# Performance work log

Hardware: AMD Instinct MI355X
Metric: run time of the kernel (lower is better)

The kernel has to match this reference:

```python
import jax, jax.numpy as jnp
import numpy as np

N = 100000
E = 400000
G = 2000  # number of graphs in batch
IN_DIM = 32
H = 192
L = 4
EPS = 1e-5


def setup_inputs() -> dict:
    key = jax.random.key(0)
    ks = jax.random.split(key, 20)
    x = jax.random.normal(ks[0], (N, IN_DIM), jnp.float32)
    edge_src = jax.random.randint(ks[1], (E,), 0, N, jnp.int32)
    edge_dst = jax.random.randint(ks[2], (E,), 0, N, jnp.int32)
    batch = jnp.sort(jax.random.randint(ks[3], (N,), 0, G, jnp.int32))
    s_in = 1.0 / np.sqrt(IN_DIM)
    s_h = 1.0 / np.sqrt(H)
    return {
        "x": x,
        "edge_src": edge_src,
        "edge_dst": edge_dst,
        "batch": batch,
        # layer 0 (in_dim -> H); weights stored [in, out]
        "Wrel0": jax.random.uniform(ks[4], (IN_DIM, H), jnp.float32, -s_in, s_in),
        "brel0": jax.random.uniform(ks[5], (H,), jnp.float32, -s_in, s_in),
        "Wroot0": jax.random.uniform(ks[6], (IN_DIM, H), jnp.float32, -s_in, s_in),
        # layers 1..3 stacked (H -> H)
        "Wrel": jax.random.uniform(ks[7], (L - 1, H, H), jnp.float32, -s_h, s_h),
        "brel": jax.random.uniform(ks[8], (L - 1, H), jnp.float32, -s_h, s_h),
        "Wroot": jax.random.uniform(ks[9], (L - 1, H, H), jnp.float32, -s_h, s_h),
        # batchnorm affine params for all 4 layers
        "gamma": jnp.ones((L, H), jnp.float32),
        "beta": jnp.zeros((L, H), jnp.float32),
        # head MLP and output
        "Wh1": jax.random.uniform(ks[10], (H, H), jnp.float32, -s_h, s_h),
        "bh1": jax.random.uniform(ks[11], (H,), jnp.float32, -s_h, s_h),
        "Wh2": jax.random.uniform(ks[12], (H, H), jnp.float32, -s_h, s_h),
        "bh2": jax.random.uniform(ks[13], (H,), jnp.float32, -s_h, s_h),
        "Wout": jax.random.uniform(ks[14], (H, 1), jnp.float32, -s_h, s_h),
        "bout": jax.random.uniform(ks[15], (1,), jnp.float32, -s_h, s_h),
    }


def _rel_conv(x, edge_src, edge_dst, Wrel, brel, Wroot):
    # message: lin_rel(x_j); applying the linear at node level first is the
    # same math as per-edge (linear commutes with gather) and cheaper.
    h = x @ Wrel + brel                      # [N, out]
    agg = jax.ops.segment_sum(h[edge_src], edge_dst, num_segments=N)
    return agg + x @ Wroot


def _bn_relu(h, g, b):
    # BatchNorm1d in training mode: batch stats over node dim, biased var
    mu = h.mean(axis=0)
    var = jnp.var(h, axis=0)
    h = (h - mu) * jax.lax.rsqrt(var + EPS) * g + b
    return jax.nn.relu(h)


def reference(x, edge_src, edge_dst, batch, Wrel0, brel0, Wroot0,
              Wrel, brel, Wroot, gamma, beta, Wh1, bh1, Wh2, bh2, Wout, bout):
    h = _bn_relu(_rel_conv(x, edge_src, edge_dst, Wrel0, brel0, Wroot0),
                 gamma[0], beta[0])
    for i in range(L - 1):
        h = _bn_relu(_rel_conv(h, edge_src, edge_dst, Wrel[i], brel[i], Wroot[i]),
                     gamma[i + 1], beta[i + 1])
    # global mean pool over graphs
    sums = jax.ops.segment_sum(h, batch, num_segments=G)          # [G, H]
    cnt = jax.ops.segment_sum(jnp.ones((N,), h.dtype), batch, num_segments=G)
    g = sums / jnp.maximum(cnt, 1.0)[:, None]
    # head MLP (dropout is identity at eval) + output linear
    g = jax.nn.relu(g @ Wh1 + bh1) @ Wh2 + bh2
    return g @ Wout + bout                                        # [G, 1]
```

## Files before the change

### kernel.cpp

```cpp
#include <hip/hip_runtime.h>

#define HDIM 192
#define EPS 1e-5f

typedef __attribute__((ext_vector_type(8))) _Float16 half8;
typedef __attribute__((ext_vector_type(4))) float floatx4;

__device__ __forceinline__ float h2f(ushort u) {
    union { ushort u; _Float16 h; } c; c.u = u; return (float)c.h;
}
__device__ __forceinline__ ushort f2h(float x) {
    _Float16 h = (_Float16)x;
    union { _Float16 h; ushort u; } c; c.h = h; return c.u;
}
__device__ __forceinline__ uint4 pack8(const ushort* h) {
    uint4 p;
    p.x = h[0] | ((uint)h[1] << 16); p.y = h[2] | ((uint)h[3] << 16);
    p.z = h[4] | ((uint)h[5] << 16); p.w = h[6] | ((uint)h[7] << 16);
    return p;
}

__device__ __forceinline__ void gload_lds16(const ushort* g, ushort* l) {
    __builtin_amdgcn_global_load_lds(
        (const __attribute__((address_space(1))) unsigned int*)g,
        (__attribute__((address_space(3))) unsigned int*)l, 16, 0, 0);
}

template<int M>
__device__ __forceinline__ void waitv() {
    if constexpr (M == 0)      asm volatile("s_waitcnt vmcnt(0)" ::: "memory");
    else if constexpr (M == 3) asm volatile("s_waitcnt vmcnt(3)" ::: "memory");
    else if constexpr (M == 7) asm volatile("s_waitcnt vmcnt(7)" ::: "memory");
    else                       asm volatile("s_waitcnt vmcnt(8)" ::: "memory");
}


struct PrepArgs {
    const float* src[6];
    ushort*      dst[6];
    int K[6];
    int off[7];
};

__global__ __launch_bounds__(256) void prep_all_k(PrepArgs a)
{
    int idx = blockIdx.x * 256 + threadIdx.x;
    if (idx >= a.off[6]) return;
    int i = 0;
    #pragma unroll
    for (int t = 1; t < 6; ++t) if (idx >= a.off[t]) i = t;
    int r = idx - a.off[i];
    int K = a.K[i];
    int perMat = (K >> 5) * 12 * 64;
    int mat = r / perMat;
    r -= mat * perMat;
    int lane = r & 63;
    int ct = (r >> 6) % 12;
    int kc = r / (12 * 64);
    int col = ct * 16 + (lane & 15);
    int kb  = kc * 32 + (lane >> 4) * 8;
    const float* Wm = a.src[i] + (size_t)mat * K * HDIM;
    ushort* base = a.dst[i] + (size_t)mat * K * HDIM;
    size_t o = (size_t)kc * 6144 + (size_t)(ct * 64 + lane) * 8;
    #pragma unroll
    for (int j = 0; j < 8; ++j)
        base[o + j] = f2h(Wm[(size_t)(kb + j) * HDIM + col]);
}

__global__ __launch_bounds__(256) void conv_half_k(
    const float* __restrict__ src, ushort* __restrict__ dst, int R, int C)
{
    int OC = C >> 3;
    int idx = blockIdx.x * 256 + threadIdx.x;
    if (idx >= R * OC) return;
    int r = idx / OC;
    int o = idx - r * OC;
    float4 v0 = ((const float4*)(src + (size_t)r * C + o * 8))[0];
    float4 v1 = ((const float4*)(src + (size_t)r * C + o * 8))[1];
    float v[8] = {v0.x, v0.y, v0.z, v0.w, v1.x, v1.y, v1.z, v1.w};
    ushort h[8];
    #pragma unroll
    for (int t = 0; t < 8; ++t) h[t] = f2h(v[t]);
    *(uint4*)(dst + (size_t)r * C + o * 8) = pack8(h);
}

template<bool DUAL, bool RELU, bool DEG, bool STATS, int NCH>
__global__ __launch_bounds__(256, 4) void gemm_mfma_k(
    const ushort* __restrict__ A1h, const ushort* __restrict__ W1f,
    const ushort* __restrict__ A2h, const ushort* __restrict__ W2f,
    const float* __restrict__ degf, const float* __restrict__ bias,
    ushort* __restrict__ C, float* __restrict__ stats, int N, int K)
{
    __shared__ float sstat[2][HDIM];
    __shared__ __align__(16) ushort smem[12800];
    const int tid  = threadIdx.x;
    const int wave = tid >> 6;
    const int lane = tid & 63;
    const int row0 = blockIdx.x * 64;
    const int m16 = lane & 15;
    const int g4  = lane >> 4;

    if (STATS && tid < HDIM) { sstat[0][tid] = 0.f; sstat[1][tid] = 0.f; }

    int srow = row0 + (tid >> 2); if (srow >= N) srow = N - 1;
    const size_t soff = (size_t)srow * K + (size_t)(tid & 3) * 8;

    const int nkc = K >> 5;

    auto stageA = [&](int c, int slot) {
        bool ph = DUAL && (c >= nkc);
        int kc = ph ? c - nkc : c;
        const ushort* g = (ph ? A2h : A1h) + soff + kc * 32;
        gload_lds16(g, smem + slot * 2048 + wave * 512);
    };
    auto loadB = [&](int c, half8* b) {
        bool ph = DUAL && (c >= nkc);
        int kc = ph ? c - nkc : c;
        const ushort* Bp = (ph ? W2f : W1f) + (size_t)kc * 6144
                         + (size_t)(wave * 192 + lane) * 8;
        #pragma unroll
        for (int ct = 0; ct < 3; ++ct)
            b[ct] = *(const half8*)(Bp + ct * 512);
    };

    floatx4 acc[4][3];
    #pragma unroll
    for (int s = 0; s < 4; ++s)
        #pragma unroll
        for (int ct = 0; ct < 3; ++ct) acc[s][ct] = (floatx4){0.f, 0.f, 0.f, 0.f};

    auto compute = [&](int slot, const half8* b) {
        const ushort* aB = smem + slot * 2048 + m16 * 32 + g4 * 8;
        half8 a[4];
        #pragma unroll
        for (int s = 0; s < 4; ++s)
            a[s] = *(const half8*)(aB + s * 512);
        #pragma unroll
        for (int ct = 0; ct < 3; ++ct)
            #pragma unroll
            for (int s = 0; s < 4; ++s)
                acc[s][ct] = __builtin_amdgcn_mfma_f32_16x16x32_f16(a[s], b[ct], acc[s][ct], 0, 0, 0);
    };

    half8 breg[3][3];
    stageA(0, 0); stageA(1, 1);
    if constexpr (NCH >= 3) stageA(2, 2);
    loadB(0, breg[0]); loadB(1, breg[1]);

    #pragma unroll
    for (int c = 0; c < NCH; ++c) {
        if (c + 3 < NCH) stageA(c + 3, (c + 3) % 5);
        if (c + 2 < NCH) loadB(c + 2, breg[(c + 2) % 3]);
        const int rem = NCH - 1 - c;
        if      (rem >= 3) waitv<8>();
        else if (rem == 2) waitv<7>();
        else if (rem == 1) waitv<3>();
        else               waitv<0>();
        __builtin_amdgcn_s_barrier();
        __builtin_amdgcn_sched_barrier(0);
        compute(c % 5, breg[c % 3]);
    }

    __syncthreads();
    #pragma unroll
    for (int ct = 0; ct < 3; ++ct) {
        int col = wave * 48 + ct * 16 + m16;
        float bv = bias ? bias[col] : 0.f;
        float lsum = 0.f, lsq = 0.f;
        #pragma unroll
        for (int s = 0; s < 4; ++s) {
            #pragma unroll
            for (int reg = 0; reg < 4; ++reg) {
                int rloc = s * 16 + g4 * 4 + reg;
                int rr = row0 + rloc;
                int rrc = rr < N ? rr : N - 1;
                float v = acc[s][ct][reg] + (DEG ? degf[rrc] * bv : bv);
                if (STATS && rr < N) { lsum += v; lsq += v * v; }
                if (RELU) v = fmaxf(v, 0.f);
                smem[rloc * 200 + col] = f2h(v);
            }
        }
        if (STATS) {
            lsum += __shfl_xor(lsum, 16); lsum += __shfl_xor(lsum, 32);
            lsq  += __shfl_xor(lsq, 16);  lsq  += __shfl_xor(lsq, 32);
            if (g4 == 0) {
                atomicAdd(&sstat[0][col], lsum);
                atomicAdd(&sstat[1][col], lsq);
            }
        }
    }
    __syncthreads();
    {
        int rowsLeft = N - row0; if (rowsLeft > 64) rowsLeft = 64;
        int lim = rowsLeft * 24;
        ushort* Cb = C + (size_t)row0 * HDIM;
        #pragma unroll
        for (int k = 0; k < 6; ++k) {
            int u = tid + k * 256;
            if (u < lim) {
                int r  = u / 24;
                int c8 = (u - r * 24) * 8;
                *(uint4*)(Cb + (size_t)u * 8) =
                    *(const uint4*)(smem + r * 200 + c8);
            }
        }
    }
    if (STATS) {
        if (tid < HDIM) {
            atomicAdd(&stats[tid], sstat[0][tid]);
            atomicAdd(&stats[HDIM + tid], sstat[1][tid]);
        }
    }
}

__global__ __launch_bounds__(256) void hist_k(
    const int* __restrict__ dst, int* __restrict__ deg, int E)
{
    int e = blockIdx.x * 256 + threadIdx.x;
    if (e < E) atomicAdd(&deg[dst[e]], 1);
}

__global__ __launch_bounds__(256) void block_sum_k(
    const int* __restrict__ deg, int* __restrict__ bsum, int N)
{
    __shared__ int s[256];
    int t = threadIdx.x;
    int n = blockIdx.x * 256 + t;
    s[t] = (n < N) ? deg[n] : 0;
    __syncthreads();
    for (int off = 128; off > 0; off >>= 1) {
        if (t < off) s[t] += s[t + off];
        __syncthreads();
    }
    if (t == 0) bsum[blockIdx.x] = s[0];
}

__global__ __launch_bounds__(512) void scan_bsum_k(int* __restrict__ bsum, int nb)
{
    __shared__ int s[512];
    int t = threadIdx.x;
    int v = (t < nb) ? bsum[t] : 0;
    s[t] = v;
    __syncthreads();
    for (int off = 1; off < 512; off <<= 1) {
        int u = (t >= off) ? s[t - off] : 0;
        __syncthreads();
        s[t] += u;
        __syncthreads();
    }
    if (t < nb) bsum[t] = s[t] - v;
}

__global__ __launch_bounds__(256) void row_ptr_k(
    const int* __restrict__ deg, const int* __restrict__ bsum,
    int* __restrict__ row_ptr, int* __restrict__ cursor,
    float* __restrict__ degf, int N, int E)
{
    __shared__ int s[256];
    int t = threadIdx.x;
    int n = blockIdx.x * 256 + t;
    int v = (n < N) ? deg[n] : 0;
    s[t] = v;
    __syncthreads();
    for (int off = 1; off < 256; off <<= 1) {
        int u = (t >= off) ? s[t - off] : 0;
        __syncthreads();
        s[t] += u;
        __syncthreads();
    }
    int ex = s[t] - v + bsum[blockIdx.x];
    if (n < N) {
        row_ptr[n] = ex;
        cursor[n]  = ex;
        degf[n]    = (float)v;
    }
    if (blockIdx.x == 0 && t == 0) row_ptr[N] = E;
}

__global__ __launch_bounds__(256) void fill_k(
    const int* __restrict__ src, const int* __restrict__ dst,
    int* __restrict__ cursor, int* __restrict__ col, int E)
{
    int e = blockIdx.x * 256 + threadIdx.x;
    if (e < E) {
        int p = atomicAdd(&cursor[dst[e]], 1);
        col[p] = src[e];
    }
}

__global__ __launch_bounds__(256) void gather_h_k(
    const ushort* __restrict__ xh, const int* __restrict__ row_ptr,
    const int* __restrict__ col, ushort* __restrict__ gh, int N, int K)
{
    int OC = K >> 3;
    int idx = blockIdx.x * 256 + threadIdx.x;
    if (idx >= N * OC) return;
    int n = idx / OC;
    int o = idx - n * OC;
    const ushort* hp = xh + o * 8;
    int j0 = row_ptr[n], j1 = row_ptr[n + 1];
    float acc[8] = {0.f,0.f,0.f,0.f,0.f,0.f,0.f,0.f};
    auto addrow = [&](uint4 hv) {
        uint hu[4] = {hv.x, hv.y, hv.z, hv.w};
        #pragma unroll
        for (int t = 0; t < 4; ++t) {
            acc[2*t]   += h2f((ushort)(hu[t] & 0xffffu));
            acc[2*t+1] += h2f((ushort)(hu[t] >> 16));
        }
    };
    int j = j0;
    for (; j + 3 < j1; j += 4) {
        int s0 = col[j], s1 = col[j+1], s2 = col[j+2], s3 = col[j+3];
        uint4 v0 = *(const uint4*)(hp + (size_t)s0 * K);
        uint4 v1 = *(const uint4*)(hp + (size_t)s1 * K);
        uint4 v2 = *(const uint4*)(hp + (size_t)s2 * K);
        uint4 v3 = *(const uint4*)(hp + (size_t)s3 * K);
        addrow(v0); addrow(v1); addrow(v2); addrow(v3);
    }
    for (; j < j1; ++j)
        addrow(*(const uint4*)(hp + (size_t)col[j] * K));
    ushort oh[8];
    #pragma unroll
    for (int t = 0; t < 8; ++t) oh[t] = f2h(acc[t]);
    *(uint4*)(gh + (size_t)n * K + o * 8) = pack8(oh);
}

__global__ __launch_bounds__(256) void gather_bn_k(
    const ushort* __restrict__ h, const float* __restrict__ stats,
    const float* __restrict__ gamma, const float* __restrict__ beta,
    float invN, const int* __restrict__ row_ptr, const int* __restrict__ col,
    ushort* __restrict__ xh, ushort* __restrict__ gh, int N)
{
    int idx = blockIdx.x * 256 + threadIdx.x;
    if (idx >= N * 24) return;
    int n = idx / 24;
    int o = idx - n * 24;
    int q = o * 8;
    float sc[8], sh[8];
    #pragma unroll
    for (int t = 0; t < 8; ++t) {
        float mu  = stats[q + t] * invN;
        float var = stats[HDIM + q + t] * invN - mu * mu;
        float s = gamma[q + t] * rsqrtf(var + EPS);
        sc[t] = s; sh[t] = beta[q + t] - mu * s;
    }
    const ushort* hp = h + q;
    {
        uint4 hv = *(const uint4*)(hp + (size_t)n * HDIM);
        uint hu[4] = {hv.x, hv.y, hv.z, hv.w};
        ushort oh[8];
        #pragma unroll
        for (int t = 0; t < 4; ++t) {
            float v0 = h2f((ushort)(hu[t] & 0xffffu));
            float v1 = h2f((ushort)(hu[t] >> 16));
            oh[2*t]   = f2h(fmaxf(v0 * sc[2*t]   + sh[2*t],   0.f));
            oh[2*t+1] = f2h(fmaxf(v1 * sc[2*t+1] + sh[2*t+1], 0.f));
        }
        *(uint4*)(xh + (size_t)n * HDIM + q) = pack8(oh);
    }
    int j0 = row_ptr[n], j1 = row_ptr[n + 1];
    float acc[8] = {0.f,0.f,0.f,0.f,0.f,0.f,0.f,0.f};
    auto addrow = [&](uint4 hv) {
        uint hu[4] = {hv.x, hv.y, hv.z, hv.w};
        #pragma unroll
        for (int t = 0; t < 4; ++t) {
            float v0 = h2f((ushort)(hu[t] & 0xffffu));
            float v1 = h2f((ushort)(hu[t] >> 16));
            acc[2*t]   += fmaxf(v0 * sc[2*t]   + sh[2*t],   0.f);
            acc[2*t+1] += fmaxf(v1 * sc[2*t+1] + sh[2*t+1], 0.f);
        }
    };
    int j = j0;
    for (; j + 3 < j1; j += 4) {
        int s0 = col[j], s1 = col[j+1], s2 = col[j+2], s3 = col[j+3];
        uint4 v0 = *(const uint4*)(hp + (size_t)s0 * HDIM);
        uint4 v1 = *(const uint4*)(hp + (size_t)s1 * HDIM);
        uint4 v2 = *(const uint4*)(hp + (size_t)s2 * HDIM);
        uint4 v3 = *(const uint4*)(hp + (size_t)s3 * HDIM);
        addrow(v0); addrow(v1); addrow(v2); addrow(v3);
    }
    for (; j < j1; ++j)
        addrow(*(const uint4*)(hp + (size_t)col[j] * HDIM));
    ushort oh[8];
    #pragma unroll
    for (int t = 0; t < 8; ++t) oh[t] = f2h(acc[t]);
    *(uint4*)(gh + (size_t)n * HDIM + q) = pack8(oh);
}

__global__ __launch_bounds__(192) void pool_bn_k(
    const ushort* __restrict__ h, const float* __restrict__ stats,
    const float* __restrict__ gamma, const float* __restrict__ beta,
    float invN, const int* __restrict__ batch,
    ushort* __restrict__ gsh, int G, int N)
{
    __shared__ int bounds[2];
    int g = blockIdx.x;
    int c = threadIdx.x;
    if (c < 2) {
        int key = g + c;
        int lo = 0, hi = N;
        while (lo < hi) {
            int mid = (lo + hi) >> 1;
            if (batch[mid] < key) lo = mid + 1; else hi = mid;
        }
        bounds[c] = lo;
    }
    __syncthreads();
    int r0 = bounds[0], r1 = bounds[1];
    float mu  = stats[c] * invN;
    float var = stats[HDIM + c] * invN - mu * mu;
    float sc  = gamma[c] * rsqrtf(var + EPS);
    float sh  = beta[c] - mu * sc;
    const ushort* base = h + c;
    float s = 0.f;
    for (int r = r0; r < r1; ++r)
        s += fmaxf(h2f(base[(size_t)r * HDIM]) * sc + sh, 0.f);
    float m = s / fmaxf((float)(r1 - r0), 1.f);
    gsh[(size_t)g * HDIM + c] = f2h(m);
}

__global__ __launch_bounds__(64) void out_dot_k(
    const ushort* __restrict__ g2h, const float* __restrict__ Wout,
    const float* __restrict__ bout, float* __restrict__ out, int G)
{
    int gi = blockIdx.x;
    int t = threadIdx.x;
    float s = 0.f;
    #pragma unroll
    for (int j = 0; j < 3; ++j) {
        int c = t + j * 64;
        s += h2f(g2h[(size_t)gi * HDIM + c]) * Wout[c];
    }
    #pragma unroll
    for (int off = 32; off > 0; off >>= 1) s += __shfl_down(s, off, 64);
    if (t == 0) out[gi] = s + bout[0];
}

extern "C" void kernel_launch(void* const* d_in, const int* in_sizes, int n_in,
                              void* d_out, int out_size, void* d_ws, size_t ws_size,
                              hipStream_t stream)
{
    const float* x      = (const float*)d_in[0];
    const int*   esrc   = (const int*)d_in[1];
    const int*   edst   = (const int*)d_in[2];
    const int*   batch  = (const int*)d_in[3];
    const float* Wrel0  = (const float*)d_in[4];
    const float* brel0  = (const float*)d_in[5];
    const float* Wroot0 = (const float*)d_in[6];
    const float* Wrel   = (const float*)d_in[7];
    const float* brel   = (const float*)d_in[8];
    const float* Wroot  = (const float*)d_in[9];
    const float* gamma  = (const float*)d_in[10];
    const float* beta   = (const float*)d_in[11];
    const float* Wh1    = (const float*)d_in[12];
    const float* bh1    = (const float*)d_in[13];
    const float* Wh2    = (const float*)d_in[14];
    const float* bh2    = (const float*)d_in[15];
    const float* Wout   = (const float*)d_in[16];
    const float* bout   = (const float*)d_in[17];
    float* out = (float*)d_out;

    const int N  = in_sizes[3];
    const int E  = in_sizes[1];
    const int K0 = in_sizes[0] / N;
    const int G  = out_size;
    const int nBlocks = (N + 255) / 256;
    const float invN = 1.0f / (float)N;

    char* p = (char*)d_ws;
    auto carve = [&](size_t bytes) -> void* {
        void* r = (void*)p; p += (bytes + 255) & ~(size_t)255; return r;
    };
    ushort* bufa_h= (ushort*)carve((size_t)N * HDIM * 2);
    ushort* xh    = (ushort*)carve((size_t)N * HDIM * 2);
    ushort* gh    = (ushort*)carve((size_t)N * HDIM * 2);
    ushort* gsh   = (ushort*)carve((size_t)G * HDIM * 2);
    ushort* g1h   = (ushort*)carve((size_t)G * HDIM * 2);
    ushort* g2h   = (ushort*)carve((size_t)G * HDIM * 2);
    int*    deg   = (int*)   carve((size_t)N * 4);
    float*  bnsums= (float*) carve(4 * 2 * HDIM * 4);
    size_t  zspan = (char*)(bnsums + 4 * 2 * HDIM) - (char*)deg;
    float*  degf  = (float*) carve((size_t)N * 4);
    int*    row_ptr=(int*)   carve((size_t)(N + 1) * 4);
    int*    cursor= (int*)   carve((size_t)N * 4);
    int*    col   = (int*)   carve((size_t)E * 4);
    int*    bsum  = (int*)   carve((size_t)nBlocks * 4);
    ushort* Wrel0f= (ushort*)carve((size_t)K0 * HDIM * 2);
    ushort* Wroot0f=(ushort*)carve((size_t)K0 * HDIM * 2);
    ushort* Wrelf = (ushort*)carve((size_t)3 * HDIM * HDIM * 2);
    ushort* Wrootf= (ushort*)carve((size_t)3 * HDIM * HDIM * 2);
    ushort* Wh1f  = (ushort*)carve((size_t)HDIM * HDIM * 2);
    ushort* Wh2f  = (ushort*)carve((size_t)HDIM * HDIM * 2);

    dim3 b256(256);
    const int eBlocks = (E + 255) / 256;
    const int gemmN = (N + 63) / 64;
    const int gemmG = (G + 63) / 64;

    {
        PrepArgs a;
        int t0 = (K0 >> 5) * 12 * 64;
        int t1 = (HDIM >> 5) * 12 * 64;
        a.src[0] = Wrel0;  a.dst[0] = Wrel0f;  a.K[0] = K0;
        a.src[1] = Wroot0; a.dst[1] = Wroot0f; a.K[1] = K0;
        a.src[2] = Wrel;   a.dst[2] = Wrelf;   a.K[2] = HDIM;
        a.src[3] = Wroot;  a.dst[3] = Wrootf;  a.K[3] = HDIM;
        a.src[4] = Wh1;    a.dst[4] = Wh1f;    a.K[4] = HDIM;
        a.src[5] = Wh2;    a.dst[5] = Wh2f;    a.K[5] = HDIM;
        a.off[0] = 0;
        a.off[1] = a.off[0] + t0;
        a.off[2] = a.off[1] + t0;
        a.off[3] = a.off[2] + 3 * t1;
        a.off[4] = a.off[3] + 3 * t1;
        a.off[5] = a.off[4] + t1;
        a.off[6] = a.off[5] + t1;
        prep_all_k<<<(a.off[6] + 255) / 256, b256, 0, stream>>>(a);
    }
    conv_half_k<<<((N * (K0 >> 3)) + 255) / 256, b256, 0, stream>>>(x, xh, N, K0);

    hipMemsetAsync(deg, 0, zspan, stream);
    hist_k<<<eBlocks, b256, 0, stream>>>(edst, deg, E);
    block_sum_k<<<nBlocks, b256, 0, stream>>>(deg, bsum, N);
    scan_bsum_k<<<1, dim3(512), 0, stream>>>(bsum, nBlocks);
    row_ptr_k<<<nBlocks, b256, 0, stream>>>(deg, bsum, row_ptr, cursor, degf, N, E);
    fill_k<<<eBlocks, b256, 0, stream>>>(esrc, edst, cursor, col, E);

    gather_h_k<<<((N * (K0 >> 3)) + 255) / 256, b256, 0, stream>>>(
        xh, row_ptr, col, gh, N, K0);
    gemm_mfma_k<true, false, true, true, 2><<<gemmN, b256, 0, stream>>>(
        gh, Wrel0f, xh, Wroot0f, degf, brel0, bufa_h, bnsums, N, K0);

    for (int l = 1; l < 4; ++l) {
        const ushort* Wrf = Wrelf  + (size_t)(l - 1) * HDIM * HDIM;
        const ushort* Wtf = Wrootf + (size_t)(l - 1) * HDIM * HDIM;
        const float*  br  = brel   + (size_t)(l - 1) * HDIM;
        gather_bn_k<<<(N * 24 + 255) / 256, b256, 0, stream>>>(
            bufa_h, bnsums + (l - 1) * 2 * HDIM,
            gamma + (l - 1) * HDIM, beta + (l - 1) * HDIM, invN,
            row_ptr, col, xh, gh, N);
        gemm_mfma_k<true, false, true, true, 12><<<gemmN, b256, 0, stream>>>(
            gh, Wrf, xh, Wtf, degf, br, bufa_h, bnsums + l * 2 * HDIM, N, HDIM);
    }

    pool_bn_k<<<G, dim3(192), 0, stream>>>(
        bufa_h, bnsums + 3 * 2 * HDIM, gamma + 3 * HDIM, beta + 3 * HDIM,
        invN, batch, gsh, G, N);

    gemm_mfma_k<false, true, false, false, 6><<<gemmG, b256, 0, stream>>>(
        gsh, Wh1f, nullptr, nullptr, nullptr, bh1, g1h, nullptr, G, HDIM);
    gemm_mfma_k<false, false, false, false, 6><<<gemmG, b256, 0, stream>>>(
        g1h, Wh2f, nullptr, nullptr, nullptr, bh2, g2h, nullptr, G, HDIM);
    out_dot_k<<<G, dim3(64), 0, stream>>>(g2h, Wout, bout, out, G);
}
```

Measured before the change: 531.9 us.

## Stage full padded A slabs into LDS once instead of a K-chunk pipeline

```diff
diff --git a/kernel.cpp b/kernel.cpp
--- a/kernel.cpp
+++ b/kernel.cpp
@@ -26,13 +26,7 @@
         (__attribute__((address_space(3))) unsigned int*)l, 16, 0, 0);
 }
 
-template<int M>
-__device__ __forceinline__ void waitv() {
-    if constexpr (M == 0)      asm volatile("s_waitcnt vmcnt(0)" ::: "memory");
-    else if constexpr (M == 3) asm volatile("s_waitcnt vmcnt(3)" ::: "memory");
-    else if constexpr (M == 7) asm volatile("s_waitcnt vmcnt(7)" ::: "memory");
-    else                       asm volatile("s_waitcnt vmcnt(8)" ::: "memory");
-}
+#define WAITV0() asm volatile("s_waitcnt vmcnt(0)" ::: "memory")
 
 
 struct PrepArgs {
@@ -84,15 +78,23 @@
     *(uint4*)(dst + (size_t)r * C + o * 8) = pack8(h);
 }
 
-template<bool DUAL, bool RELU, bool DEG, bool STATS, int NCH>
-__global__ __launch_bounds__(256, 4) void gemm_mfma_k(
+template<bool DUAL, bool RELU, bool DEG, bool STATS, int NKC>
+__global__ __launch_bounds__(256, 3) void gemm_mfma_k(
     const ushort* __restrict__ A1h, const ushort* __restrict__ W1f,
     const ushort* __restrict__ A2h, const ushort* __restrict__ W2f,
     const float* __restrict__ degf, const float* __restrict__ bias,
     ushort* __restrict__ C, float* __restrict__ stats, int N, int K)
 {
+    constexpr int KR   = NKC * 32;
+    constexpr int RS   = KR + 8;
+    constexpr int SLAB = 64 * RS;
+    constexpr int NINSTR = SLAB / 512;
+    constexpr int NCH  = DUAL ? 2 * NKC : NKC;
+    constexpr int SMEMU = ((DUAL ? 2 * SLAB : SLAB) > 12800)
+                            ? (DUAL ? 2 * SLAB : SLAB) : 12800;
+
     __shared__ float sstat[2][HDIM];
-    __shared__ __align__(16) ushort smem[12800];
+    __shared__ __align__(16) ushort smem[SMEMU];
     const int tid  = threadIdx.x;
     const int wave = tid >> 6;
     const int lane = tid & 63;
@@ -102,20 +104,28 @@
 
     if (STATS && tid < HDIM) { sstat[0][tid] = 0.f; sstat[1][tid] = 0.f; }
 
-    int srow = row0 + (tid >> 2); if (srow >= N) srow = N - 1;
-    const size_t soff = (size_t)srow * K + (size_t)(tid & 3) * 8;
-
-    const int nkc = K >> 5;
-
-    auto stageA = [&](int c, int slot) {
-        bool ph = DUAL && (c >= nkc);
-        int kc = ph ? c - nkc : c;
-        const ushort* g = (ph ? A2h : A1h) + soff + kc * 32;
-        gload_lds16(g, smem + slot * 2048 + wave * 512);
+    auto stage = [&](const ushort* Ab, int slabOff) {
+        #pragma unroll
+        for (int i = wave; i < NINSTR; i += 4) {
+            int slotB = i * 1024 + lane * 16;
+            int r   = slotB / (RS * 2);
+            int off = slotB - r * (RS * 2);
+            if (off >= KR * 2) off = KR * 2 - 16;
+            int rr = row0 + r; if (rr >= N) rr = N - 1;
+            gload_lds16(Ab + (size_t)rr * KR + (off >> 1),
+                        smem + slabOff + i * 512);
+        }
     };
+
+    stage(A1h, 0);
+    if constexpr (DUAL) stage(A2h, SLAB);
+    WAITV0();
+    __builtin_amdgcn_s_barrier();
+    __builtin_amdgcn_sched_barrier(0);
+
     auto loadB = [&](int c, half8* b) {
-        bool ph = DUAL && (c >= nkc);
-        int kc = ph ? c - nkc : c;
+        bool ph = DUAL && (c >= NKC);
+        int kc = ph ? c - NKC : c;
         const ushort* Bp = (ph ? W2f : W1f) + (size_t)kc * 6144
                          + (size_t)(wave * 192 + lane) * 8;
         #pragma unroll
@@ -129,36 +139,24 @@
         #pragma unroll
         for (int ct = 0; ct < 3; ++ct) acc[s][ct] = (floatx4){0.f, 0.f, 0.f, 0.f};
 
-    auto compute = [&](int slot, const half8* b) {
-        const ushort* aB = smem + slot * 2048 + m16 * 32 + g4 * 8;
+    half8 bA[3], bB[3];
+    loadB(0, bA);
+    #pragma unroll
+    for (int c = 0; c < NCH; ++c) {
+        if (c + 1 < NCH) loadB(c + 1, (c & 1) ? bA : bB);
+        const int base = (DUAL && c >= NKC) ? SLAB : 0;
+        const int kc   = (DUAL && c >= NKC) ? c - NKC : c;
+        const ushort* aB = smem + base + m16 * RS + kc * 32 + g4 * 8;
         half8 a[4];
         #pragma unroll
         for (int s = 0; s < 4; ++s)
-            a[s] = *(const half8*)(aB + s * 512);
+            a[s] = *(const half8*)(aB + s * 16 * RS);
+        const half8* bu = (c & 1) ? bB : bA;
         #pragma unroll
         for (int ct = 0; ct < 3; ++ct)
             #pragma unroll
             for (int s = 0; s < 4; ++s)
-                acc[s][ct] = __builtin_amdgcn_mfma_f32_16x16x32_f16(a[s], b[ct], acc[s][ct], 0, 0, 0);
-    };
-
-    half8 breg[3][3];
-    stageA(0, 0); stageA(1, 1);
-    if constexpr (NCH >= 3) stageA(2, 2);
-    loadB(0, breg[0]); loadB(1, breg[1]);
-
-    #pragma unroll
-    for (int c = 0; c < NCH; ++c) {
-        if (c + 3 < NCH) stageA(c + 3, (c + 3) % 5);
-        if (c + 2 < NCH) loadB(c + 2, breg[(c + 2) % 3]);
-        const int rem = NCH - 1 - c;
-        if      (rem >= 3) waitv<8>();
-        else if (rem == 2) waitv<7>();
-        else if (rem == 1) waitv<3>();
-        else               waitv<0>();
-        __builtin_amdgcn_s_barrier();
-        __builtin_amdgcn_sched_barrier(0);
-        compute(c % 5, breg[c % 3]);
+                acc[s][ct] = __builtin_amdgcn_mfma_f32_16x16x32_f16(a[s], bu[ct], acc[s][ct], 0, 0, 0);
     }
 
     __syncthreads();
@@ -527,7 +525,7 @@
 
     gather_h_k<<<((N * (K0 >> 3)) + 255) / 256, b256, 0, stream>>>(
         xh, row_ptr, col, gh, N, K0);
-    gemm_mfma_k<true, false, true, true, 2><<<gemmN, b256, 0, stream>>>(
+    gemm_mfma_k<true, false, true, true, 1><<<gemmN, b256, 0, stream>>>(
         gh, Wrel0f, xh, Wroot0f, degf, brel0, bufa_h, bnsums, N, K0);
 
     for (int l = 1; l < 4; ++l) {
@@ -538,7 +536,7 @@
             bufa_h, bnsums + (l - 1) * 2 * HDIM,
             gamma + (l - 1) * HDIM, beta + (l - 1) * HDIM, invN,
             row_ptr, col, xh, gh, N);
-        gemm_mfma_k<true, false, true, true, 12><<<gemmN, b256, 0, stream>>>(
+        gemm_mfma_k<true, false, true, true, 6><<<gemmN, b256, 0, stream>>>(
             gh, Wrf, xh, Wtf, degf, br, bufa_h, bnsums + l * 2 * HDIM, N, HDIM);
     }
 
```

Result: slower. 551.8 us (+3.7%).
